# Performance work log

Hardware: AMD Instinct MI355X
Metric: run time of the kernel (lower is better)

Reference implementation:

```python
import jax, jax.numpy as jnp
import numpy as np

SIGNAL_DIM = 64   # D
STATE_DIM = 64    # N
SEQ_LEN = 16384   # L
BATCH = 16


def _init_dplr_hippo(state_dim):
    """NumPy port of init_DPLR_HiPPO(signal_dim=1, state_dim). Returns Lambda,(N,) P,(N,) B,(N,1) complex64."""
    n = np.arange(state_dim, dtype=np.float64)
    A = np.zeros((state_dim, state_dim))
    for k in range(state_dim):
        A[k:, k] = np.sqrt(2.0 * np.arange(k, state_dim) + 1.0) * np.sqrt(2.0 * k + 1.0)
        A[k, k] = k + 1
    A = -A
    P = np.sqrt(n + 0.5)
    SI = A + P[:, None] * P[None, :]
    diag = np.diagonal(SI).copy()
    S = SI - np.diag(diag)
    eigvals, V = np.linalg.eigh(S * -1j)   # S*-1j is Hermitian
    Lam = diag + 1j * eigvals
    Vc = V.conj().T
    Pc = Vc @ P.astype(np.complex128)
    B = np.sqrt(2.0 * n + 1.0)[:, None]    # (N, 1): signal_dim=1, tied across channels
    Bc = Vc @ B.astype(np.complex128)
    return Lam.astype(np.complex64), Pc.astype(np.complex64), Bc.astype(np.complex64)


def _ri(x):
    # complex -> (..., 2) float32, matching torch.view_as_real parameter storage
    return jnp.stack([jnp.real(x), jnp.imag(x)], axis=-1).astype(jnp.float32)


def _to_c(x):
    return jax.lax.complex(x[..., 0], x[..., 1])


def setup_inputs() -> dict:
    key = jax.random.key(0)
    ku, kc1, kc2, kd, ks = jax.random.split(key, 5)
    Lam, P, B = _init_dplr_hippo(STATE_DIM)
    C = (jax.random.normal(kc1, (SIGNAL_DIM, STATE_DIM)) +
         1j * jax.random.normal(kc2, (SIGNAL_DIM, STATE_DIM))).astype(jnp.complex64)
    return {
        "u": jax.random.normal(ku, (BATCH, SEQ_LEN, SIGNAL_DIM), dtype=jnp.float32),
        "Lambda_ri": _ri(jnp.asarray(Lam)),      # (N, 2)
        "P_ri": _ri(jnp.asarray(P)),             # (N, 2)
        "B_ri": _ri(jnp.asarray(B)),             # (N, 1, 2)
        "C_ri": _ri(C),                          # (D, N, 2)
        "D_param": jax.random.normal(kd, (SIGNAL_DIM,), dtype=jnp.float32),
        "log_step": jnp.log(jax.random.uniform(ks, (1,), minval=0.001, maxval=0.1)).astype(jnp.float32),
    }


def reference(u, Lambda_ri, P_ri, B_ri, C_ri, D_param, log_step):
    Lam = _to_c(Lambda_ri)   # (N,)
    P = _to_c(P_ri)          # (N,)
    B = _to_c(B_ri)          # (N, 1)
    C = _to_c(C_ri)          # (D, N)
    L = u.shape[-2]

    step = jnp.exp(log_step)                                  # (1,)
    Omega = jnp.exp(-2j * jnp.pi * (jnp.arange(L) / L))       # (L,) roots of unity
    g = (2.0 / step) * ((1.0 - Omega) / (1.0 + Omega))        # (L,)

    # Batched Cauchy kernel: k_ab[l] = sum_n a_n * b_n / (g_l - Lambda_n)
    cauchy = 1.0 / (g[:, None] - Lam[None, :])                # (L, N)
    a0 = jnp.conj(C)        # (D, N)
    a1 = jnp.conj(P)        # (N,)
    b0 = B[:, 0]            # (N,)  == B.T row (signal_dim=1)
    b1 = P                  # (N,)
    k00 = jnp.einsum('dn,n,ln->dl', a0, b0, cauchy)
    k01 = jnp.einsum('dn,n,ln->dl', a0, b1, cauchy)
    k10 = jnp.einsum('n,n,ln->l', a1, b0, cauchy)
    k11 = jnp.einsum('n,n,ln->l', a1, b1, cauchy)

    evaluated = (2.0 / (1.0 + Omega)) * (k00 - k01 * (1.0 / (1.0 + k11)) * k10)  # (D, L)
    K = jnp.fft.ifft(evaluated, axis=-1).T.real               # (L, D) conv kernel

    # FFT convolution along time axis (zero-pad to 2L, linear convolution)
    ud = jnp.fft.rfft(jnp.pad(u, ((0, 0), (0, L), (0, 0))), axis=-2)
    Kd = jnp.fft.rfft(jnp.pad(K, ((0, L), (0, 0))), axis=-2)
    y = jnp.fft.irfft(ud * Kd, n=2 * L, axis=-2)[..., :L, :]
    return y + D_param * u
```

## Files before the change

kernel.cpp:

```cpp
#include <hip/hip_runtime.h>
#include <math.h>

#define MF 16384
#define HALF 8192

__device__ __forceinline__ float2 cmul(float2 a, float2 b){ return make_float2(a.x*b.x - a.y*b.y, a.x*b.y + a.y*b.x); }
__device__ __forceinline__ float2 cmulc(float2 a, float2 b){ return make_float2(a.x*b.x + a.y*b.y, a.y*b.x - a.x*b.y); }
__device__ __forceinline__ int rho4(int v){ return ((v & 3) << 2) | (v >> 2); }
__device__ __forceinline__ int sob(int k){
    return (rho4(k & 15) << 10) | (rho4((k >> 4) & 15) << 6) | (rho4((k >> 8) & 15) << 2) | (k >> 12);
}
__device__ __forceinline__ int ph(int e){ return e ^ ((e >> 4) & 3) ^ (((e >> 6) & 3) << 2); }

__device__ __forceinline__ void bf4f(float2&a,float2&b,float2&c,float2&d){
    float t0x=a.x+c.x, t0y=a.y+c.y, t2x=a.x-c.x, t2y=a.y-c.y;
    float t1x=b.x+d.x, t1y=b.y+d.y, t3x=b.x-d.x, t3y=b.y-d.y;
    a=make_float2(t0x+t1x,t0y+t1y);
    b=make_float2(t2x+t3y,t2y-t3x);
    c=make_float2(t0x-t1x,t0y-t1y);
    d=make_float2(t2x-t3y,t2y+t3x);
}
__device__ __forceinline__ void bf4i(float2&a,float2&b,float2&c,float2&d){
    float t0x=a.x+c.x, t0y=a.y+c.y, t2x=a.x-c.x, t2y=a.y-c.y;
    float t1x=b.x+d.x, t1y=b.y+d.y, t3x=b.x-d.x, t3y=b.y-d.y;
    a=make_float2(t0x+t1x,t0y+t1y);
    b=make_float2(t2x-t3y,t2y+t3x);
    c=make_float2(t0x-t1x,t0y-t1y);
    d=make_float2(t2x+t3y,t2y-t3x);
}

#define W16_1 make_float2(0.92387953251128674f, -0.38268343236508978f)
#define W16_2 make_float2(0.70710678118654752f, -0.70710678118654752f)
#define W16_3 make_float2(0.38268343236508978f, -0.92387953251128674f)
#define W16_6 make_float2(-0.70710678118654752f, -0.70710678118654752f)
#define W16_9 make_float2(-0.92387953251128674f, 0.38268343236508978f)

__device__ __forceinline__ void dft16_fwd(float2* x){
    bf4f(x[0],x[4],x[8],x[12]);
    bf4f(x[1],x[5],x[9],x[13]);
    bf4f(x[2],x[6],x[10],x[14]);
    bf4f(x[3],x[7],x[11],x[15]);
    x[5]=cmul(x[5],W16_1);  x[9]=cmul(x[9],W16_2);   x[13]=cmul(x[13],W16_3);
    x[6]=cmul(x[6],W16_2);  { float2 t=x[10]; x[10]=make_float2(t.y,-t.x); } x[14]=cmul(x[14],W16_6);
    x[7]=cmul(x[7],W16_3);  x[11]=cmul(x[11],W16_6); x[15]=cmul(x[15],W16_9);
    bf4f(x[0],x[1],x[2],x[3]);
    bf4f(x[4],x[5],x[6],x[7]);
    bf4f(x[8],x[9],x[10],x[11]);
    bf4f(x[12],x[13],x[14],x[15]);
}
__device__ __forceinline__ void dft16_inv(float2* x){
    bf4i(x[0],x[1],x[2],x[3]);
    bf4i(x[4],x[5],x[6],x[7]);
    bf4i(x[8],x[9],x[10],x[11]);
    bf4i(x[12],x[13],x[14],x[15]);
    x[5]=cmulc(x[5],W16_1); x[9]=cmulc(x[9],W16_2);  x[13]=cmulc(x[13],W16_3);
    x[6]=cmulc(x[6],W16_2); { float2 t=x[10]; x[10]=make_float2(-t.y,t.x); } x[14]=cmulc(x[14],W16_6);
    x[7]=cmulc(x[7],W16_3); x[11]=cmulc(x[11],W16_6); x[15]=cmulc(x[15],W16_9);
    bf4i(x[0],x[4],x[8],x[12]);
    bf4i(x[1],x[5],x[9],x[13]);
    bf4i(x[2],x[6],x[10],x[14]);
    bf4i(x[3],x[7],x[11],x[15]);
}

template<bool INV>
__device__ __forceinline__ void tw0_apply(float2* x, float2 w1){
    float2 w2=cmul(w1,w1), w4=cmul(w2,w2), w8=cmul(w4,w4);
    float2 w3=cmul(w2,w1), w5=cmul(w4,w1), w6=cmul(w4,w2), w7=cmul(w4,w3);
    float2 w9=cmul(w8,w1), w10=cmul(w8,w2), w11=cmul(w8,w3), w12=cmul(w8,w4);
    float2 w13=cmul(w8,w5), w14=cmul(w8,w6), w15=cmul(w8,w7);
    if (!INV){
        x[1]=cmul(x[1],w4);   x[2]=cmul(x[2],w8);   x[3]=cmul(x[3],w12);
        x[4]=cmul(x[4],w1);   x[5]=cmul(x[5],w5);   x[6]=cmul(x[6],w9);
        x[7]=cmul(x[7],w13);  x[8]=cmul(x[8],w2);   x[9]=cmul(x[9],w6);
        x[10]=cmul(x[10],w10);x[11]=cmul(x[11],w14);x[12]=cmul(x[12],w3);
        x[13]=cmul(x[13],w7); x[14]=cmul(x[14],w11);x[15]=cmul(x[15],w15);
    } else {
        x[1]=cmulc(x[1],w4);   x[2]=cmulc(x[2],w8);   x[3]=cmulc(x[3],w12);
        x[4]=cmulc(x[4],w1);   x[5]=cmulc(x[5],w5);   x[6]=cmulc(x[6],w9);
        x[7]=cmulc(x[7],w13);  x[8]=cmulc(x[8],w2);   x[9]=cmulc(x[9],w6);
        x[10]=cmulc(x[10],w10);x[11]=cmulc(x[11],w14);x[12]=cmulc(x[12],w3);
        x[13]=cmulc(x[13],w7); x[14]=cmulc(x[14],w11);x[15]=cmulc(x[15],w15);
    }
}

template<bool INV>
__device__ __forceinline__ void pass0(float2* A, float2 w1g, int tid){
    float2 x[16];
    int base = ph(tid);
    #pragma unroll
    for(int m=0;m<16;++m) x[m] = A[base + (m<<10)];
    if(!INV){ dft16_fwd(x); tw0_apply<false>(x, w1g); }
    else { tw0_apply<true>(x, w1g); dft16_inv(x); }
    #pragma unroll
    for(int m=0;m<16;++m) A[base + (m<<10)] = x[m];
}

template<bool INV>
__device__ __forceinline__ void pass1(float2* A, const float2* basP1, int tid){
    float2 x[16];
    int i1 = tid & 63;
    int B = (tid >> 6) << 10;
    int i1x = i1 ^ ((i1 >> 4) & 3);
    int b0 = B | i1x;
    int b1 = B | 64 | (i1x ^ 4);
    int b2 = B | 128 | (i1x ^ 8);
    int b3 = B | 192 | (i1x ^ 12);
    x[0]=A[b0];     x[1]=A[b1];     x[2]=A[b2];     x[3]=A[b3];
    x[4]=A[b0+256]; x[5]=A[b1+256]; x[6]=A[b2+256]; x[7]=A[b3+256];
    x[8]=A[b0+512]; x[9]=A[b1+512]; x[10]=A[b2+512];x[11]=A[b3+512];
    x[12]=A[b0+768];x[13]=A[b1+768];x[14]=A[b2+768];x[15]=A[b3+768];
    float2 w1 = basP1[i1];
    if(!INV){ dft16_fwd(x); tw0_apply<false>(x, w1); }
    else { tw0_apply<true>(x, w1); dft16_inv(x); }
    A[b0]=x[0];     A[b1]=x[1];     A[b2]=x[2];     A[b3]=x[3];
    A[b0+256]=x[4]; A[b1+256]=x[5]; A[b2+256]=x[6]; A[b3+256]=x[7];
    A[b0+512]=x[8]; A[b1+512]=x[9]; A[b2+512]=x[10];A[b3+512]=x[11];
    A[b0+768]=x[12];A[b1+768]=x[13];A[b2+768]=x[14];A[b3+768]=x[15];
}

template<bool INV>
__device__ __forceinline__ void pass2(float2* A, const float2* basP2, int tid){
    float2 x[16];
    int q = tid >> 2, j2 = tid & 3;
    int qb = q << 6, qa = q & 3;
    int c0 = qb | (j2 ^ 0);
    int c1 = qb | 16 | (j2 ^ 1);
    int c2 = qb | 32 | (j2 ^ 2);
    int c3 = qb | 48 | (j2 ^ 3);
    int r0 = (qa ^ 0) << 2, r1 = (qa ^ 1) << 2, r2 = (qa ^ 2) << 2, r3 = (qa ^ 3) << 2;
    x[0]=A[c0+r0];  x[1]=A[c0+r1];  x[2]=A[c0+r2];  x[3]=A[c0+r3];
    x[4]=A[c1+r0];  x[5]=A[c1+r1];  x[6]=A[c1+r2];  x[7]=A[c1+r3];
    x[8]=A[c2+r0];  x[9]=A[c2+r1];  x[10]=A[c2+r2]; x[11]=A[c2+r3];
    x[12]=A[c3+r0]; x[13]=A[c3+r1]; x[14]=A[c3+r2]; x[15]=A[c3+r3];
    float2 w1 = basP2[j2];
    if(!INV){ dft16_fwd(x); tw0_apply<false>(x, w1); }
    else { tw0_apply<true>(x, w1); dft16_inv(x); }
    A[c0+r0]=x[0];  A[c0+r1]=x[1];  A[c0+r2]=x[2];  A[c0+r3]=x[3];
    A[c1+r0]=x[4];  A[c1+r1]=x[5];  A[c1+r2]=x[6];  A[c1+r3]=x[7];
    A[c2+r0]=x[8];  A[c2+r1]=x[9];  A[c2+r2]=x[10]; A[c2+r3]=x[11];
    A[c3+r0]=x[12]; A[c3+r1]=x[13]; A[c3+r2]=x[14]; A[c3+r3]=x[15];
}

template<bool INV>
__device__ __forceinline__ void pass3(float2* A, int tid){
    int sgm = ((tid>>2)&3) ^ (((tid>>4)&3)<<2);
    #pragma unroll
    for(int rr=0; rr<4; ++rr){
        int base = (tid<<2) | (rr<<12);
        float2 a=A[(base|0)^sgm], b=A[(base|1)^sgm], c=A[(base|2)^sgm], d=A[(base|3)^sgm];
        if(!INV) bf4f(a,b,c,d); else bf4i(a,b,c,d);
        A[(base|0)^sgm]=a; A[(base|1)^sgm]=b; A[(base|2)^sgm]=c; A[(base|3)^sgm]=d;
    }
}

__device__ __forceinline__ float2 pw_slot(float2 Zk, float2 Zm, float4 kd, float2 w){
    Zm.y = -Zm.y;
    float2 Ue = make_float2(0.5f*(Zk.x+Zm.x), 0.5f*(Zk.y+Zm.y));
    float2 dd = make_float2(Zk.x-Zm.x, Zk.y-Zm.y);
    float2 Uo = make_float2(0.5f*dd.y, -0.5f*dd.x);
    float2 t2 = cmul(w, Uo);
    float2 X0 = make_float2(Ue.x+t2.x, Ue.y+t2.y);
    float2 X1 = make_float2(Ue.x-t2.x, Ue.y-t2.y);
    float2 Y0 = cmul(X0, make_float2(kd.x,kd.y));
    float2 Y1 = cmul(X1, make_float2(kd.z,kd.w));
    float2 Ey = make_float2(0.5f*(Y0.x+Y1.x), 0.5f*(Y0.y+Y1.y));
    float2 Dy = make_float2(Y0.x-Y1.x, Y0.y-Y1.y);
    float2 Oy = cmulc(Dy, w);
    return make_float2(Ey.x - 0.5f*Oy.y, Ey.y + 0.5f*Oy.x);
}
template<int I>
__device__ __forceinline__ float2 wslot(float2 wb){
    const float r2 = 0.70710678118654752f;
    if (I==0) return wb;
    if (I==1) return make_float2((wb.x+wb.y)*r2, (wb.y-wb.x)*r2);
    if (I==2) return make_float2(wb.y, -wb.x);
    return make_float2((wb.y-wb.x)*r2, -(wb.x+wb.y)*r2);
}
__device__ __forceinline__ void quadgeo(int v, int& pb, int& px, int& qs, float2& wb){
    int qq = rho4((v>>8)&15) | (rho4((v>>4)&15)<<4) | (rho4(v&15)<<8);
    qs = qq << 2;
    pb = qs ^ (((qq>>4)&3)<<2);
    px = (qq>>2)&3;
    float vf = (float)v * (1.0f/16384.0f);
    wb = make_float2(cospif(vf), -sinpif(vf));
}
template<int MODE>
__device__ __forceinline__ void pw_pair(float2* A, const float4* Kd,
        int pba, int pxa, float2 wba, int qsa,
        int pbb, int pxb, float2 wbb, int qsb){
    float2 za[4], zb[4];
    za[0]=A[pba+(0^pxa)]; za[1]=A[pba+(1^pxa)]; za[2]=A[pba+(2^pxa)]; za[3]=A[pba+(3^pxa)];
    zb[0]=A[pbb+(0^pxb)]; zb[1]=A[pbb+(1^pxb)]; zb[2]=A[pbb+(2^pxb)]; zb[3]=A[pbb+(3^pxb)];
    bf4f(za[0],za[1],za[2],za[3]);
    bf4f(zb[0],zb[1],zb[2],zb[3]);
    float4 ka0=Kd[qsa+0], ka1=Kd[qsa+1], ka2=Kd[qsa+2], ka3=Kd[qsa+3];
    float4 kb0=Kd[qsb+0], kb1=Kd[qsb+1], kb2=Kd[qsb+2], kb3=Kd[qsb+3];
    float2 wa[4], wz[4];
    if (MODE == 0){
        wa[0]=pw_slot(za[0], zb[3], ka0, wslot<0>(wba));
        wa[1]=pw_slot(za[1], zb[2], ka1, wslot<1>(wba));
        wa[2]=pw_slot(za[2], zb[1], ka2, wslot<2>(wba));
        wa[3]=pw_slot(za[3], zb[0], ka3, wslot<3>(wba));
        wz[0]=pw_slot(zb[0], za[3], kb0, wslot<0>(wbb));
        wz[1]=pw_slot(zb[1], za[2], kb1, wslot<1>(wbb));
        wz[2]=pw_slot(zb[2], za[1], kb2, wslot<2>(wbb));
        wz[3]=pw_slot(zb[3], za[0], kb3, wslot<3>(wbb));
    } else {
        wa[0]=pw_slot(za[0], zb[0], ka0, wslot<0>(wba));
        wa[1]=pw_slot(za[1], zb[3], ka1, wslot<1>(wba));
        wa[2]=pw_slot(za[2], zb[2], ka2, wslot<2>(wba));
        wa[3]=pw_slot(za[3], zb[1], ka3, wslot<3>(wba));
        wz[0]=wa[0]; wz[1]=wa[1]; wz[2]=wa[2]; wz[3]=wa[3];
    }
    bf4i(wa[0],wa[1],wa[2],wa[3]);
    bf4i(wz[0],wz[1],wz[2],wz[3]);
    A[pba+(0^pxa)]=wa[0]; A[pba+(1^pxa)]=wa[1]; A[pba+(2^pxa)]=wa[2]; A[pba+(3^pxa)]=wa[3];
    A[pbb+(0^pxb)]=wz[0]; A[pbb+(1^pxb)]=wz[1]; A[pbb+(2^pxb)]=wz[2]; A[pbb+(3^pxb)]=wz[3];
}

__global__ __launch_bounds__(1024) void k_evalinit(const float2* __restrict__ Lam, const float2* __restrict__ P,
        const float2* __restrict__ Bc, const float2* __restrict__ C,
        const float* __restrict__ log_step, float2* __restrict__ E, float2* __restrict__ baseg) {
    __shared__ float2 bTs[16][64];
    __shared__ float2 pTs[16][64];
    __shared__ float2 S10s[16], S11s[16];
    __shared__ float2 C_l[64][65];
    __shared__ float2 tile[16][65];
    int tid = threadIdx.x;
    if (blockIdx.x >= 256){
        const double TP = 6.2831853071795864769;
        double a = -TP * (double)tid / 16384.0;
        baseg[tid] = make_float2((float)cos(a), (float)sin(a));
        return;
    }
    int l0 = blockIdx.x * 64;
    float step = expf(log_step[0]);
    {
        int dq = tid >> 6, n = tid & 63;
        #pragma unroll
        for (int p = 0; p < 4; ++p) { int dd = dq + p * 16; C_l[n][dd] = C[dd * 64 + n]; }
    }
    __syncthreads();
    int w = tid >> 6;
    int lane = tid & 63;
    for (int p = 0; p < 4; ++p) {
        int l = l0 + p * 16 + w;
        float lf = (float)l * (1.0f / 16384.0f);
        float s2 = sinpif(lf), c2 = cospif(lf);
        float2 q1 = make_float2(2.0f*c2*c2, -2.0f*s2*c2);
        {
            int n = lane;
            float2 q2 = make_float2(4.0f*s2*s2, 4.0f*s2*c2);
            float2 ln = Lam[n];
            float2 lq = cmul(ln, q1);
            float2 den = make_float2(q2.x - step*lq.x, q2.y - step*lq.y);
            float idn = step / (den.x*den.x + den.y*den.y);
            float2 T = make_float2(den.x*idn, -den.y*idn);
            float2 bn = Bc[n], pn = P[n];
            float2 bT = cmul(bn, T), pT = cmul(pn, T);
            bTs[w][n] = bT; pTs[w][n] = pT;
            float2 s10 = make_float2(pn.x*bT.x + pn.y*bT.y, pn.x*bT.y - pn.y*bT.x);
            float2 s11 = make_float2(pn.x*pT.x + pn.y*pT.y, pn.x*pT.y - pn.y*pT.x);
            #pragma unroll
            for (int off = 32; off > 0; off >>= 1) {
                s10.x += __shfl_xor(s10.x, off);
                s10.y += __shfl_xor(s10.y, off);
                s11.x += __shfl_xor(s11.x, off);
                s11.y += __shfl_xor(s11.y, off);
            }
            if (n == 0) { S10s[w] = s10; S11s[w] = s11; }
        }
        __syncthreads();
        {
            int d = lane;
            float2 S00 = make_float2(0.f, 0.f), S01 = make_float2(0.f, 0.f);
            #pragma unroll 8
            for (int n = 0; n < 64; ++n) {
                float2 cn = C_l[n][d];
                float2 bT = bTs[w][n];
                float2 pT = pTs[w][n];
                S00.x += cn.x*bT.x + cn.y*bT.y;  S00.y += cn.x*bT.y - cn.y*bT.x;
                S01.x += cn.x*pT.x + cn.y*pT.y;  S01.y += cn.x*pT.y - cn.y*pT.x;
            }
            float2 S10 = S10s[w], S11 = S11s[w];
            float2 k11 = cmul(q1, S11); k11.x += 1.0f;
            float2 k10q = cmul(q1, S10);
            float ik = 1.0f / (k11.x*k11.x + k11.y*k11.y);
            float2 quo = make_float2((k10q.x*k11.x + k10q.y*k11.y) * ik,
                                     (k10q.y*k11.x - k10q.x*k11.y) * ik);
            float2 corr = cmul(S01, quo);
            tile[w][d] = make_float2(2.0f*(S00.x - corr.x), 2.0f*(S00.y - corr.y));
        }
        __syncthreads();
        {
            int lo = tid & 15, dq = tid >> 4;
            E[(size_t)dq * MF + l0 + p * 16 + lo] = tile[lo][dq];
        }
        __syncthreads();
    }
}

union MidShm {
    struct { float2 A[MF]; float2 basP1[64]; float2 basP2[4]; } p;
    float t[256][65];
};

__global__ __launch_bounds__(1024, 4) void k_mid(const float2* __restrict__ E, float4* __restrict__ Ktab,
        const float2* __restrict__ baseg, const float* __restrict__ u, float* __restrict__ uT) {
    __shared__ MidShm sh;
    int tid = threadIdx.x;
    if (blockIdx.x >= 64){
        int cid = blockIdx.x - 64;
        int b = cid >> 6, t0c = (cid & 63) << 8;
        const float* ub = u + ((size_t)(b * MF + t0c)) * 64;
        #pragma unroll
        for (int it = 0; it < 16; ++it){
            int tl = it * 16 + (tid >> 6), dl = tid & 63;
            sh.t[tl][dl] = ub[(size_t)tl * 64 + dl];
        }
        __syncthreads();
        float* dst = uT + (size_t)b * 64 * MF + t0c;
        #pragma unroll
        for (int it = 0; it < 16; ++it){
            int dd = (tid >> 8) + it * 4, tl = tid & 255;
            dst[(size_t)dd * MF + tl] = sh.t[tl][dd];
        }
        return;
    }
    float2* A = sh.p.A;
    float2* basP1 = sh.p.basP1;
    float2* basP2 = sh.p.basP2;
    float2 w1g = baseg[tid];
    if (tid < 64) basP1[tid] = baseg[tid << 4];
    if (tid < 4)  basP2[tid] = baseg[tid << 8];
    int d = blockIdx.x;
    const float2* Ed = E + (size_t)d * MF;
    #pragma unroll
    for (int r = 0; r < 16; ++r) { int l = tid + (r << 10); A[ph(sob(l))] = Ed[l]; }
    __syncthreads();
    pass3<true>(A, tid); __syncthreads();
    pass2<true>(A, basP2, tid); __syncthreads();
    pass1<true>(A, basP1, tid); __syncthreads();
    pass0<true>(A, w1g, tid); __syncthreads();
    const float s = 1.0f / (float)MF;
    float2 rv[8];
    #pragma unroll
    for (int r = 0; r < 8; ++r) {
        int t = tid + (r << 10);
        rv[r] = make_float2(A[ph(2*t)].x * s, A[ph(2*t+1)].x * s);
    }
    __syncthreads();
    int pht = ph(tid);
    #pragma unroll
    for (int r = 0; r < 16; ++r) A[pht + (r << 10)] = (r < 8) ? rv[r] : make_float2(0.f, 0.f);
    __syncthreads();
    pass0<false>(A, w1g, tid); __syncthreads();
    pass1<false>(A, basP1, tid); __syncthreads();
    pass2<false>(A, basP2, tid); __syncthreads();
    pass3<false>(A, tid); __syncthreads();
    float4* Kd = Ktab + (size_t)d * MF;
    int Cbits = (rho4(tid >> 6) << 4) | (rho4((tid >> 2) & 15) << 8) | ((tid & 3) << 12);
    const float ksc = 1.0f / (float)MF;
    #pragma unroll
    for (int r = 0; r < 16; ++r) {
        int k = Cbits | rho4(r);
        int kp = (MF - k) & (MF - 1);
        int p = sob(kp);
        float kf = (float)k * (1.0f / 16384.0f);
        float2 w = make_float2(cospif(kf), -sinpif(kf));
        float2 Zk = A[pht + (r << 10)];
        float2 Zm = A[ph(p)]; Zm.y = -Zm.y;
        float2 Ue = make_float2(0.5f*(Zk.x + Zm.x), 0.5f*(Zk.y + Zm.y));
        float2 dd = make_float2(Zk.x - Zm.x, Zk.y - Zm.y);
        float2 Uo = make_float2(0.5f*dd.y, -0.5f*dd.x);
        float2 t2 = cmul(w, Uo);
        Kd[tid + (r << 10)] = make_float4((Ue.x + t2.x)*ksc, (Ue.y + t2.y)*ksc,
                                          (Ue.x - t2.x)*ksc, (Ue.y - t2.y)*ksc);
    }
}

template<bool TRANS>
__global__ __launch_bounds__(1024, 4) void k_conv(const float* __restrict__ u, const float* __restrict__ uT,
        const float4* __restrict__ Ktab, const float* __restrict__ Dp,
        float* __restrict__ yT, float* __restrict__ yout, const float2* __restrict__ baseg) {
    __shared__ float2 A[MF];
    __shared__ float2 basP1[64];
    __shared__ float2 basP2[4];
    int tid = threadIdx.x;
    float2 w1g = baseg[tid];
    if (tid < 64) basP1[tid] = baseg[tid << 4];
    if (tid < 4)  basP2[tid] = baseg[tid << 8];
    int bid = blockIdx.x;
    int vb = ((bid & 7) << 7) | (bid >> 3);
    int d = vb >> 4, b = vb & 15;
    int bd = (b << 6) | d;
    int base = ph(tid);
    const float2* src = (const float2*)(uT + (size_t)bd * MF);
    const float* ub = u + ((size_t)b * MF) * 64 + d;
    {
        float2 x[16];
        #pragma unroll
        for (int m = 0; m < 16; ++m){
            if (m < 8){
                if (TRANS) x[m] = src[tid + (m << 10)];
                else { int t = tid + (m << 10); x[m] = make_float2(ub[(size_t)(2*t)*64], ub[(size_t)(2*t+1)*64]); }
            } else x[m] = make_float2(0.f, 0.f);
        }
        dft16_fwd(x);
        tw0_apply<false>(x, w1g);
        #pragma unroll
        for (int m = 0; m < 16; ++m) A[base + (m << 10)] = x[m];
    }
    __syncthreads();
    pass1<false>(A, basP1, tid); __syncthreads();
    pass2<false>(A, basP2, tid); __syncthreads();
    const float4* Kd = Ktab + (size_t)d * MF;
    if (tid != 0){
        int pb0,px0,qs0; float2 wb0; quadgeo(2*tid,      pb0,px0,qs0,wb0);
        int pb1,px1,qs1; float2 wb1; quadgeo(2*tid+1,    pb1,px1,qs1,wb1);
        int pb2,px2,qs2; float2 wb2; quadgeo(4096-2*tid, pb2,px2,qs2,wb2);
        int pb3,px3,qs3; float2 wb3; quadgeo(4095-2*tid, pb3,px3,qs3,wb3);
        pw_pair<0>(A, Kd, pb0,px0,wb0,qs0, pb2,px2,wb2,qs2);
        pw_pair<0>(A, Kd, pb1,px1,wb1,qs1, pb3,px3,wb3,qs3);
    } else {
        int pb0,px0,qs0; float2 wb0; quadgeo(0,    pb0,px0,qs0,wb0);
        int pb1,px1,qs1; float2 wb1; quadgeo(1,    pb1,px1,qs1,wb1);
        int pb2,px2,qs2; float2 wb2; quadgeo(4095, pb2,px2,qs2,wb2);
        int pb3,px3,qs3; float2 wb3; quadgeo(2048, pb3,px3,qs3,wb3);
        pw_pair<1>(A, Kd, pb0,px0,wb0,qs0, pb0,px0,wb0,qs0);
        pw_pair<0>(A, Kd, pb1,px1,wb1,qs1, pb2,px2,wb2,qs2);
        pw_pair<0>(A, Kd, pb3,px3,wb3,qs3, pb3,px3,wb3,qs3);
    }
    __syncthreads();
    pass2<true>(A, basP2, tid); __syncthreads();
    pass1<true>(A, basP1, tid); __syncthreads();
    {
        float2 x[16];
        #pragma unroll
        for (int m = 0; m < 16; ++m) x[m] = A[base + (m << 10)];
        tw0_apply<true>(x, w1g);
        dft16_inv(x);
        float Dd = Dp[d];
        if (TRANS){
            float2* dst = (float2*)(yT + (size_t)bd * MF);
            #pragma unroll
            for (int m = 0; m < 8; ++m){
                float2 s2 = src[tid + (m << 10)];
                dst[tid + (m << 10)] = make_float2(x[m].x + Dd * s2.x, x[m].y + Dd * s2.y);
            }
        } else {
            float* yb = yout + ((size_t)b * MF) * 64 + d;
            #pragma unroll
            for (int m = 0; m < 8; ++m){
                int t = tid + (m << 10);
                yb[(size_t)(2*t)*64]   = x[m].x + Dd * ub[(size_t)(2*t)*64];
                yb[(size_t)(2*t+1)*64] = x[m].y + Dd * ub[(size_t)(2*t+1)*64];
            }
        }
    }
}

__global__ void k_out(const float* __restrict__ yT, float* __restrict__ y) {
    __shared__ float tile[64][65];
    int b = blockIdx.y, t0 = blockIdx.x * 64, tid = threadIdx.x;
    #pragma unroll
    for (int k2 = 0; k2 < 16; ++k2) {
        int idx = tid + k2 * 256;
        int dl = idx >> 6, tl = idx & 63;
        tile[dl][tl] = yT[((size_t)b * 64 + dl) * MF + t0 + tl];
    }
    __syncthreads();
    #pragma unroll
    for (int k2 = 0; k2 < 16; ++k2) {
        int idx = tid + k2 * 256;
        int tl = idx >> 6, dl = idx & 63;
        y[((size_t)(b * MF + t0 + tl)) * 64 + dl] = tile[dl][tl];
    }
}

extern "C" void kernel_launch(void* const* d_in, const int* in_sizes, int n_in,
                              void* d_out, int out_size, void* d_ws, size_t ws_size,
                              hipStream_t stream) {
    const float*  u   = (const float*)d_in[0];
    const float2* Lam = (const float2*)d_in[1];
    const float2* P   = (const float2*)d_in[2];
    const float2* Bc  = (const float2*)d_in[3];
    const float2* C   = (const float2*)d_in[4];
    const float*  Dp  = (const float*)d_in[5];
    const float*  ls  = (const float*)d_in[6];
    float* y = (float*)d_out;
    char* ws = (char*)d_ws;

    size_t off = 0;
    float2* baseg = (float2*)(ws + off); off += (size_t)1024 * sizeof(float2);
    float2* E     = (float2*)(ws + off); off += (size_t)64 * MF * sizeof(float2);
    float4* Ktab  = (float4*)(ws + off); off += (size_t)64 * MF * sizeof(float4);
    float*  uT    = (float*) (ws + off); off += (size_t)1024 * MF * sizeof(float);
    float*  yT    = (float*) (ws + off); off += (size_t)1024 * MF * sizeof(float);
    bool trans = (ws_size >= off);

    k_evalinit<<<257, 1024, 0, stream>>>(Lam, P, Bc, C, ls, E, baseg);
    k_mid<<<trans ? 1088 : 64, 1024, 0, stream>>>(E, Ktab, baseg, u, uT);

    if (trans) {
        k_conv<true><<<1024, 1024, 0, stream>>>(u, uT, Ktab, Dp, yT, y, baseg);
        k_out<<<dim3(MF / 64, 16), 256, 0, stream>>>(yT, y);
    } else {
        k_conv<false><<<1024, 1024, 0, stream>>>(u, nullptr, Ktab, Dp, nullptr, y, baseg);
    }
}
```

Baseline: 306.6 us.

## Use precomputed twiddle tables and restructure pointwise stage with full radix-4 passes

Replaces the per-thread twiddle computation in FFT passes 1 and 2 with full precomputed twiddle tables in shared memory, generated once in the init kernel. The conv kernel's fused radix-4 pointwise pair step is replaced by an explicit pass3 forward, a per-element real-FFT untangle and kernel multiply with Ktab prefetched into registers, then pass3 inverse. The explicit launch bound occupancy hint of 4 is removed. This trades fewer twiddle multiplies for more shared memory, extra barriers and two extra LDS passes, and the higher register use may lower occupancy.

```diff
diff --git a/kernel.cpp b/kernel.cpp
--- a/kernel.cpp
+++ b/kernel.cpp
@@ -96,7 +96,7 @@
 }
 
 template<bool INV>
-__device__ __forceinline__ void pass1(float2* A, const float2* basP1, int tid){
+__device__ __forceinline__ void pass1(float2* A, const float2* tw1s, int tid){
     float2 x[16];
     int i1 = tid & 63;
     int B = (tid >> 6) << 10;
@@ -109,9 +109,15 @@
     x[4]=A[b0+256]; x[5]=A[b1+256]; x[6]=A[b2+256]; x[7]=A[b3+256];
     x[8]=A[b0+512]; x[9]=A[b1+512]; x[10]=A[b2+512];x[11]=A[b3+512];
     x[12]=A[b0+768];x[13]=A[b1+768];x[14]=A[b2+768];x[15]=A[b3+768];
-    float2 w1 = basP1[i1];
-    if(!INV){ dft16_fwd(x); tw0_apply<false>(x, w1); }
-    else { tw0_apply<true>(x, w1); dft16_inv(x); }
+    if(!INV){
+        dft16_fwd(x);
+        #pragma unroll
+        for(int j=1;j<16;++j) x[j] = cmul(x[j], tw1s[(j<<6)+i1]);
+    } else {
+        #pragma unroll
+        for(int j=1;j<16;++j) x[j] = cmulc(x[j], tw1s[(j<<6)+i1]);
+        dft16_inv(x);
+    }
     A[b0]=x[0];     A[b1]=x[1];     A[b2]=x[2];     A[b3]=x[3];
     A[b0+256]=x[4]; A[b1+256]=x[5]; A[b2+256]=x[6]; A[b3+256]=x[7];
     A[b0+512]=x[8]; A[b1+512]=x[9]; A[b2+512]=x[10];A[b3+512]=x[11];
@@ -119,7 +125,7 @@
 }
 
 template<bool INV>
-__device__ __forceinline__ void pass2(float2* A, const float2* basP2, int tid){
+__device__ __forceinline__ void pass2(float2* A, const float2* tw2s, int tid){
     float2 x[16];
     int q = tid >> 2, j2 = tid & 3;
     int qb = q << 6, qa = q & 3;
@@ -132,9 +138,15 @@
     x[4]=A[c1+r0];  x[5]=A[c1+r1];  x[6]=A[c1+r2];  x[7]=A[c1+r3];
     x[8]=A[c2+r0];  x[9]=A[c2+r1];  x[10]=A[c2+r2]; x[11]=A[c2+r3];
     x[12]=A[c3+r0]; x[13]=A[c3+r1]; x[14]=A[c3+r2]; x[15]=A[c3+r3];
-    float2 w1 = basP2[j2];
-    if(!INV){ dft16_fwd(x); tw0_apply<false>(x, w1); }
-    else { tw0_apply<true>(x, w1); dft16_inv(x); }
+    if(!INV){
+        dft16_fwd(x);
+        #pragma unroll
+        for(int j=1;j<16;++j) x[j] = cmul(x[j], tw2s[(j<<2)+j2]);
+    } else {
+        #pragma unroll
+        for(int j=1;j<16;++j) x[j] = cmulc(x[j], tw2s[(j<<2)+j2]);
+        dft16_inv(x);
+    }
     A[c0+r0]=x[0];  A[c0+r1]=x[1];  A[c0+r2]=x[2];  A[c0+r3]=x[3];
     A[c1+r0]=x[4];  A[c1+r1]=x[5];  A[c1+r2]=x[6];  A[c1+r3]=x[7];
     A[c2+r0]=x[8];  A[c2+r1]=x[9];  A[c2+r2]=x[10]; A[c2+r3]=x[11];
@@ -153,74 +165,10 @@
     }
 }
 
-__device__ __forceinline__ float2 pw_slot(float2 Zk, float2 Zm, float4 kd, float2 w){
-    Zm.y = -Zm.y;
-    float2 Ue = make_float2(0.5f*(Zk.x+Zm.x), 0.5f*(Zk.y+Zm.y));
-    float2 dd = make_float2(Zk.x-Zm.x, Zk.y-Zm.y);
-    float2 Uo = make_float2(0.5f*dd.y, -0.5f*dd.x);
-    float2 t2 = cmul(w, Uo);
-    float2 X0 = make_float2(Ue.x+t2.x, Ue.y+t2.y);
-    float2 X1 = make_float2(Ue.x-t2.x, Ue.y-t2.y);
-    float2 Y0 = cmul(X0, make_float2(kd.x,kd.y));
-    float2 Y1 = cmul(X1, make_float2(kd.z,kd.w));
-    float2 Ey = make_float2(0.5f*(Y0.x+Y1.x), 0.5f*(Y0.y+Y1.y));
-    float2 Dy = make_float2(Y0.x-Y1.x, Y0.y-Y1.y);
-    float2 Oy = cmulc(Dy, w);
-    return make_float2(Ey.x - 0.5f*Oy.y, Ey.y + 0.5f*Oy.x);
-}
-template<int I>
-__device__ __forceinline__ float2 wslot(float2 wb){
-    const float r2 = 0.70710678118654752f;
-    if (I==0) return wb;
-    if (I==1) return make_float2((wb.x+wb.y)*r2, (wb.y-wb.x)*r2);
-    if (I==2) return make_float2(wb.y, -wb.x);
-    return make_float2((wb.y-wb.x)*r2, -(wb.x+wb.y)*r2);
-}
-__device__ __forceinline__ void quadgeo(int v, int& pb, int& px, int& qs, float2& wb){
-    int qq = rho4((v>>8)&15) | (rho4((v>>4)&15)<<4) | (rho4(v&15)<<8);
-    qs = qq << 2;
-    pb = qs ^ (((qq>>4)&3)<<2);
-    px = (qq>>2)&3;
-    float vf = (float)v * (1.0f/16384.0f);
-    wb = make_float2(cospif(vf), -sinpif(vf));
-}
-template<int MODE>
-__device__ __forceinline__ void pw_pair(float2* A, const float4* Kd,
-        int pba, int pxa, float2 wba, int qsa,
-        int pbb, int pxb, float2 wbb, int qsb){
-    float2 za[4], zb[4];
-    za[0]=A[pba+(0^pxa)]; za[1]=A[pba+(1^pxa)]; za[2]=A[pba+(2^pxa)]; za[3]=A[pba+(3^pxa)];
-    zb[0]=A[pbb+(0^pxb)]; zb[1]=A[pbb+(1^pxb)]; zb[2]=A[pbb+(2^pxb)]; zb[3]=A[pbb+(3^pxb)];
-    bf4f(za[0],za[1],za[2],za[3]);
-    bf4f(zb[0],zb[1],zb[2],zb[3]);
-    float4 ka0=Kd[qsa+0], ka1=Kd[qsa+1], ka2=Kd[qsa+2], ka3=Kd[qsa+3];
-    float4 kb0=Kd[qsb+0], kb1=Kd[qsb+1], kb2=Kd[qsb+2], kb3=Kd[qsb+3];
-    float2 wa[4], wz[4];
-    if (MODE == 0){
-        wa[0]=pw_slot(za[0], zb[3], ka0, wslot<0>(wba));
-        wa[1]=pw_slot(za[1], zb[2], ka1, wslot<1>(wba));
-        wa[2]=pw_slot(za[2], zb[1], ka2, wslot<2>(wba));
-        wa[3]=pw_slot(za[3], zb[0], ka3, wslot<3>(wba));
-        wz[0]=pw_slot(zb[0], za[3], kb0, wslot<0>(wbb));
-        wz[1]=pw_slot(zb[1], za[2], kb1, wslot<1>(wbb));
-        wz[2]=pw_slot(zb[2], za[1], kb2, wslot<2>(wbb));
-        wz[3]=pw_slot(zb[3], za[0], kb3, wslot<3>(wbb));
-    } else {
-        wa[0]=pw_slot(za[0], zb[0], ka0, wslot<0>(wba));
-        wa[1]=pw_slot(za[1], zb[3], ka1, wslot<1>(wba));
-        wa[2]=pw_slot(za[2], zb[2], ka2, wslot<2>(wba));
-        wa[3]=pw_slot(za[3], zb[1], ka3, wslot<3>(wba));
-        wz[0]=wa[0]; wz[1]=wa[1]; wz[2]=wa[2]; wz[3]=wa[3];
-    }
-    bf4i(wa[0],wa[1],wa[2],wa[3]);
-    bf4i(wz[0],wz[1],wz[2],wz[3]);
-    A[pba+(0^pxa)]=wa[0]; A[pba+(1^pxa)]=wa[1]; A[pba+(2^pxa)]=wa[2]; A[pba+(3^pxa)]=wa[3];
-    A[pbb+(0^pxb)]=wz[0]; A[pbb+(1^pxb)]=wz[1]; A[pbb+(2^pxb)]=wz[2]; A[pbb+(3^pxb)]=wz[3];
-}
-
 __global__ __launch_bounds__(1024) void k_evalinit(const float2* __restrict__ Lam, const float2* __restrict__ P,
         const float2* __restrict__ Bc, const float2* __restrict__ C,
-        const float* __restrict__ log_step, float2* __restrict__ E, float2* __restrict__ baseg) {
+        const float* __restrict__ log_step, float2* __restrict__ E,
+        float2* __restrict__ baseg, float2* __restrict__ tw1g, float2* __restrict__ tw2g) {
     __shared__ float2 bTs[16][64];
     __shared__ float2 pTs[16][64];
     __shared__ float2 S10s[16], S11s[16];
@@ -231,6 +179,12 @@
         const double TP = 6.2831853071795864769;
         double a = -TP * (double)tid / 16384.0;
         baseg[tid] = make_float2((float)cos(a), (float)sin(a));
+        double a1 = -TP * (double)((tid & 63) * rho4(tid >> 6)) / 1024.0;
+        tw1g[tid] = make_float2((float)cos(a1), (float)sin(a1));
+        if (tid < 64){
+            double a2 = -TP * (double)((tid & 3) * rho4(tid >> 2)) / 64.0;
+            tw2g[tid] = make_float2((float)cos(a2), (float)sin(a2));
+        }
         return;
     }
     int l0 = blockIdx.x * 64;
@@ -301,12 +255,13 @@
 }
 
 union MidShm {
-    struct { float2 A[MF]; float2 basP1[64]; float2 basP2[4]; } p;
+    struct { float2 A[MF]; float2 tw1s[1024]; float2 tw2s[64]; } p;
     float t[256][65];
 };
 
-__global__ __launch_bounds__(1024, 4) void k_mid(const float2* __restrict__ E, float4* __restrict__ Ktab,
-        const float2* __restrict__ baseg, const float* __restrict__ u, float* __restrict__ uT) {
+__global__ __launch_bounds__(1024) void k_mid(const float2* __restrict__ E, float4* __restrict__ Ktab,
+        const float2* __restrict__ baseg, const float2* __restrict__ tw1g, const float2* __restrict__ tw2g,
+        const float* __restrict__ u, float* __restrict__ uT) {
     __shared__ MidShm sh;
     int tid = threadIdx.x;
     if (blockIdx.x >= 64){
@@ -328,19 +283,19 @@
         return;
     }
     float2* A = sh.p.A;
-    float2* basP1 = sh.p.basP1;
-    float2* basP2 = sh.p.basP2;
+    float2* tw1s = sh.p.tw1s;
+    float2* tw2s = sh.p.tw2s;
     float2 w1g = baseg[tid];
-    if (tid < 64) basP1[tid] = baseg[tid << 4];
-    if (tid < 4)  basP2[tid] = baseg[tid << 8];
+    tw1s[tid] = tw1g[tid];
+    if (tid < 64) tw2s[tid] = tw2g[tid];
     int d = blockIdx.x;
     const float2* Ed = E + (size_t)d * MF;
     #pragma unroll
     for (int r = 0; r < 16; ++r) { int l = tid + (r << 10); A[ph(sob(l))] = Ed[l]; }
     __syncthreads();
     pass3<true>(A, tid); __syncthreads();
-    pass2<true>(A, basP2, tid); __syncthreads();
-    pass1<true>(A, basP1, tid); __syncthreads();
+    pass2<true>(A, tw2s, tid); __syncthreads();
+    pass1<true>(A, tw1s, tid); __syncthreads();
     pass0<true>(A, w1g, tid); __syncthreads();
     const float s = 1.0f / (float)MF;
     float2 rv[8];
@@ -355,8 +310,8 @@
     for (int r = 0; r < 16; ++r) A[pht + (r << 10)] = (r < 8) ? rv[r] : make_float2(0.f, 0.f);
     __syncthreads();
     pass0<false>(A, w1g, tid); __syncthreads();
-    pass1<false>(A, basP1, tid); __syncthreads();
-    pass2<false>(A, basP2, tid); __syncthreads();
+    pass1<false>(A, tw1s, tid); __syncthreads();
+    pass2<false>(A, tw2s, tid); __syncthreads();
     pass3<false>(A, tid); __syncthreads();
     float4* Kd = Ktab + (size_t)d * MF;
     int Cbits = (rho4(tid >> 6) << 4) | (rho4((tid >> 2) & 15) << 8) | ((tid & 3) << 12);
@@ -380,16 +335,17 @@
 }
 
 template<bool TRANS>
-__global__ __launch_bounds__(1024, 4) void k_conv(const float* __restrict__ u, const float* __restrict__ uT,
+__global__ __launch_bounds__(1024) void k_conv(const float* __restrict__ u, const float* __restrict__ uT,
         const float4* __restrict__ Ktab, const float* __restrict__ Dp,
-        float* __restrict__ yT, float* __restrict__ yout, const float2* __restrict__ baseg) {
+        float* __restrict__ yT, float* __restrict__ yout,
+        const float2* __restrict__ baseg, const float2* __restrict__ tw1g, const float2* __restrict__ tw2g) {
     __shared__ float2 A[MF];
-    __shared__ float2 basP1[64];
-    __shared__ float2 basP2[4];
+    __shared__ float2 tw1s[1024];
+    __shared__ float2 tw2s[64];
     int tid = threadIdx.x;
     float2 w1g = baseg[tid];
-    if (tid < 64) basP1[tid] = baseg[tid << 4];
-    if (tid < 4)  basP2[tid] = baseg[tid << 8];
+    tw1s[tid] = tw1g[tid];
+    if (tid < 64) tw2s[tid] = tw2g[tid];
     int bid = blockIdx.x;
     int vb = ((bid & 7) << 7) | (bid >> 3);
     int d = vb >> 4, b = vb & 15;
@@ -412,28 +368,45 @@
         for (int m = 0; m < 16; ++m) A[base + (m << 10)] = x[m];
     }
     __syncthreads();
-    pass1<false>(A, basP1, tid); __syncthreads();
-    pass2<false>(A, basP2, tid); __syncthreads();
+    pass1<false>(A, tw1s, tid); __syncthreads();
+    pass2<false>(A, tw2s, tid); __syncthreads();
     const float4* Kd = Ktab + (size_t)d * MF;
-    if (tid != 0){
-        int pb0,px0,qs0; float2 wb0; quadgeo(2*tid,      pb0,px0,qs0,wb0);
-        int pb1,px1,qs1; float2 wb1; quadgeo(2*tid+1,    pb1,px1,qs1,wb1);
-        int pb2,px2,qs2; float2 wb2; quadgeo(4096-2*tid, pb2,px2,qs2,wb2);
-        int pb3,px3,qs3; float2 wb3; quadgeo(4095-2*tid, pb3,px3,qs3,wb3);
-        pw_pair<0>(A, Kd, pb0,px0,wb0,qs0, pb2,px2,wb2,qs2);
-        pw_pair<0>(A, Kd, pb1,px1,wb1,qs1, pb3,px3,wb3,qs3);
-    } else {
-        int pb0,px0,qs0; float2 wb0; quadgeo(0,    pb0,px0,qs0,wb0);
-        int pb1,px1,qs1; float2 wb1; quadgeo(1,    pb1,px1,qs1,wb1);
-        int pb2,px2,qs2; float2 wb2; quadgeo(4095, pb2,px2,qs2,wb2);
-        int pb3,px3,qs3; float2 wb3; quadgeo(2048, pb3,px3,qs3,wb3);
-        pw_pair<1>(A, Kd, pb0,px0,wb0,qs0, pb0,px0,wb0,qs0);
-        pw_pair<0>(A, Kd, pb1,px1,wb1,qs1, pb2,px2,wb2,qs2);
-        pw_pair<0>(A, Kd, pb3,px3,wb3,qs3, pb3,px3,wb3,qs3);
-    }
-    __syncthreads();
-    pass2<true>(A, basP2, tid); __syncthreads();
-    pass1<true>(A, basP1, tid); __syncthreads();
+    float4 kd[16];
+    #pragma unroll
+    for (int r = 0; r < 16; ++r) kd[r] = Kd[tid + (r << 10)];
+    pass3<false>(A, tid); __syncthreads();
+    int Cbits = (rho4(tid >> 6) << 4) | (rho4((tid >> 2) & 15) << 8) | ((tid & 3) << 12);
+    float2 Wr[16];
+    #pragma unroll
+    for (int r = 0; r < 16; ++r) {
+        int k = Cbits | rho4(r);
+        int kp = (MF - k) & (MF - 1);
+        int p = sob(kp);
+        float kf = (float)k * (1.0f / 16384.0f);
+        float2 w = make_float2(cospif(kf), -sinpif(kf));
+        float2 Zk = A[base + (r << 10)];
+        float2 Zm = A[ph(p)]; Zm.y = -Zm.y;
+        float2 Ue = make_float2(0.5f*(Zk.x + Zm.x), 0.5f*(Zk.y + Zm.y));
+        float2 dd = make_float2(Zk.x - Zm.x, Zk.y - Zm.y);
+        float2 Uo = make_float2(0.5f*dd.y, -0.5f*dd.x);
+        float2 t2 = cmul(w, Uo);
+        float2 X0 = make_float2(Ue.x + t2.x, Ue.y + t2.y);
+        float2 X1 = make_float2(Ue.x - t2.x, Ue.y - t2.y);
+        float2 Y0 = cmul(X0, make_float2(kd[r].x, kd[r].y));
+        float2 Y1 = cmul(X1, make_float2(kd[r].z, kd[r].w));
+        float2 Ey = make_float2(0.5f*(Y0.x + Y1.x), 0.5f*(Y0.y + Y1.y));
+        float2 Dy = make_float2(Y0.x - Y1.x, Y0.y - Y1.y);
+        float2 Oy = cmulc(Dy, w);
+        Oy.x *= 0.5f; Oy.y *= 0.5f;
+        Wr[r] = make_float2(Ey.x - Oy.y, Ey.y + Oy.x);
+    }
+    __syncthreads();
+    #pragma unroll
+    for (int r = 0; r < 16; ++r) A[base + (r << 10)] = Wr[r];
+    __syncthreads();
+    pass3<true>(A, tid); __syncthreads();
+    pass2<true>(A, tw2s, tid); __syncthreads();
+    pass1<true>(A, tw1s, tid); __syncthreads();
     {
         float2 x[16];
         #pragma unroll
@@ -493,19 +466,21 @@
 
     size_t off = 0;
     float2* baseg = (float2*)(ws + off); off += (size_t)1024 * sizeof(float2);
+    float2* tw1g  = (float2*)(ws + off); off += (size_t)1024 * sizeof(float2);
+    float2* tw2g  = (float2*)(ws + off); off += (size_t)64 * sizeof(float2) + 512;
     float2* E     = (float2*)(ws + off); off += (size_t)64 * MF * sizeof(float2);
     float4* Ktab  = (float4*)(ws + off); off += (size_t)64 * MF * sizeof(float4);
     float*  uT    = (float*) (ws + off); off += (size_t)1024 * MF * sizeof(float);
     float*  yT    = (float*) (ws + off); off += (size_t)1024 * MF * sizeof(float);
     bool trans = (ws_size >= off);
 
-    k_evalinit<<<257, 1024, 0, stream>>>(Lam, P, Bc, C, ls, E, baseg);
-    k_mid<<<trans ? 1088 : 64, 1024, 0, stream>>>(E, Ktab, baseg, u, uT);
+    k_evalinit<<<257, 1024, 0, stream>>>(Lam, P, Bc, C, ls, E, baseg, tw1g, tw2g);
+    k_mid<<<trans ? 1088 : 64, 1024, 0, stream>>>(E, Ktab, baseg, tw1g, tw2g, u, uT);
 
     if (trans) {
-        k_conv<true><<<1024, 1024, 0, stream>>>(u, uT, Ktab, Dp, yT, y, baseg);
+        k_conv<true><<<1024, 1024, 0, stream>>>(u, uT, Ktab, Dp, yT, y, baseg, tw1g, tw2g);
         k_out<<<dim3(MF / 64, 16), 256, 0, stream>>>(yT, y);
     } else {
-        k_conv<false><<<1024, 1024, 0, stream>>>(u, nullptr, Ktab, Dp, nullptr, y, baseg);
-    }
-}
+        k_conv<false><<<1024, 1024, 0, stream>>>(u, nullptr, Ktab, Dp, nullptr, y, baseg, tw1g, tw2g);
+    }
+}
```

Result: faster. 299.8 us (-2.2%).
